# Kernel optimization log

Hardware: AMD Instinct MI355X
Metric: run time of the kernel (lower is better)

## Reference

```python
import jax, jax.numpy as jnp
import numpy as np

B, G, C, Hmlp, R = 4, 2048, 384, 1536, 96
NH = 6          # attention heads
V = 6           # number of 2D views (len(out_transform_2d))
NC = 1024       # number of clusters for segment_csr
GX = GY = 32    # grid shape per view
SCALE_FACTOR = 0.5  # args.scale_factor
COEF_PRO = 0.5      # args.coef_pro
EPS_LN = 1e-5
EPS_BN = 1e-5


def _forward(x, center1, norm1_g, norm1_b, qkv_w, proj_w, proj_b, norm2_g, norm2_b,
             fc1_w, fc1_b, fc2_w, fc2_b, ada1_w, ada1_b, ada2_w, ada2_b,
             bn3_g, bn3_b, bn3_m, bn3_v, bn2_g, bn2_b, bn2_m, bn2_v,
             norm3_g, norm3_b, a1_qkv_w, a1_proj_w, a1_proj_b,
             mask, idx_ptr, sorted_cluster_indices, cluster, flat_grid_index,
             grid_shape_x, grid_shape_y):
    B_, G1, C_ = x.shape
    hd = C_ // NH

    def ln(t, g, b):
        mu = t.mean(-1, keepdims=True)
        var = ((t - mu) ** 2).mean(-1, keepdims=True)
        return (t - mu) * jax.lax.rsqrt(var + EPS_LN) * g + b

    def bn_gelu(t, g, b, m, v):  # BatchNorm1d (eval) + GELU
        t = (t - m) * jax.lax.rsqrt(v + EPS_BN) * g + b
        return jax.nn.gelu(t, approximate=False)

    # ---- multi-head self-attention sublayer ----
    h = ln(x, norm1_g, norm1_b)
    qkv = (h @ qkv_w).reshape(B_, G1, 3, NH, hd).transpose(2, 0, 3, 1, 4)
    q, k, v = qkv[0], qkv[1], qkv[2]
    attn = jax.nn.softmax(jnp.einsum('bhqd,bhkd->bhqk', q, k) * hd ** -0.5, axis=-1)
    o = jnp.einsum('bhqk,bhkd->bhqd', attn, v).transpose(0, 2, 1, 3).reshape(B_, G1, C_)
    x = x + o @ proj_w + proj_b

    # ---- MLP + adapter sublayer ----
    h2 = ln(x, norm2_g, norm2_b)
    ffn = jax.nn.gelu(h2 @ fc1_w + fc1_b, approximate=False) @ fc2_w + fc2_b
    a = ffn @ ada1_w + ada1_b
    a = a * jax.nn.sigmoid(1.702 * a)      # QuickGELU
    ada = a @ ada2_w + ada2_b
    x = x + ffn + SCALE_FACTOR * ada

    cls_x = x[:, :1]
    pts = x[:, 1:]
    Gp = G1 - 1
    N = B_ * Gp

    # ---- 3D branch: segment_csr max/mean over clusters, gather back ----
    feat = pts.reshape(N, C_)
    fs = feat[sorted_cluster_indices]
    seg = cluster[sorted_cluster_indices]          # sorted segment ids (CSR order)
    nc = idx_ptr.shape[0] - 1
    cnt = jax.ops.segment_sum(jnp.ones((N,), feat.dtype), seg, nc)
    fsum = jax.ops.segment_sum(fs, seg, nc)
    fmax = jax.ops.segment_max(fs, seg, nc)
    fmax = jnp.where(cnt[:, None] > 0, fmax, 0.0)
    fmean = fsum / jnp.maximum(cnt, 1.0)[:, None]
    x3d = bn_gelu(fmax + fmean, bn3_g, bn3_b, bn3_m, bn3_v)[cluster].reshape(pts.shape)

    # ---- per-view 2D branch: masked attn + scatter_max/mean over grid cells ----
    dim_size = center1.shape[0] * grid_shape_x * grid_shape_y
    nviews = center1.shape[1]
    views = []
    for i in range(nviews):
        fx = pts.reshape(N, C_)
        h3 = ln(fx, norm3_g[i], norm3_b[i]).reshape(B_, Gp, C_)
        qkv1 = (h3 @ a1_qkv_w[i]).reshape(B_, Gp, 3, C_).transpose(2, 0, 1, 3)
        q1, k1, v1 = qkv1[0], qkv1[1], qkv1[2]
        s = jnp.einsum('bqd,bkd->bqk', q1, k1) * C_ ** -0.5
        s = jnp.where(mask[i][None], s, jnp.finfo(s.dtype).min)
        o1 = jnp.einsum('bqk,bkd->bqd', jax.nn.softmax(s, axis=-1), v1) @ a1_proj_w[i] + a1_proj_b[i]
        fx = o1.reshape(N, C_) + fx
        gi = flat_grid_index[i]
        gc = jax.ops.segment_sum(jnp.ones((N,), fx.dtype), gi, dim_size)
        gs = jax.ops.segment_sum(fx, gi, dim_size)
        gm = jax.ops.segment_max(fx, gi, dim_size)
        gm = jnp.where(gc[:, None] > 0, gm, 0.0)
        cell = bn_gelu(gs / jnp.maximum(gc, 1.0)[:, None] + gm,
                       bn2_g[i], bn2_b[i], bn2_m[i], bn2_v[i])
        views.append(cell[gi].reshape(pts.shape))

    # ---- cosine-similarity weighted fusion across views ----
    x_sup = jnp.stack(views, 0)                     # [V,B,G,C]
    dot = jnp.sum(x_sup * x3d[None], -1)
    nrm = jnp.linalg.norm(x_sup, axis=-1) * jnp.linalg.norm(x3d, axis=-1)[None]
    sims = (dot / jnp.maximum(nrm, 1e-8) + 1.0) / 2.0
    sims = sims / sims.sum(0, keepdims=True)
    x_sup_w = jnp.sum(x_sup * sims[..., None], 0)
    pts = pts + COEF_PRO * x_sup_w
    return jnp.concatenate([cls_x, pts], axis=1)


def setup_inputs() -> dict:
    rng = np.random.default_rng(0)
    key = jax.random.key(0)
    N = B * G
    # consistent cluster structure: every cluster non-empty
    cluster = np.concatenate([np.arange(NC), rng.integers(0, NC, N - NC)]).astype(np.int32)
    rng.shuffle(cluster)
    sorted_idx = np.argsort(cluster, kind='stable').astype(np.int32)
    counts = np.bincount(cluster, minlength=NC)
    idx_ptr = np.concatenate([[0], np.cumsum(counts)]).astype(np.int32)
    flat_grid_index = rng.integers(0, B * GX * GY, (V, N)).astype(np.int32)
    mask = (rng.random((V, G, G)) < 0.25) | np.eye(G, dtype=bool)[None]
    ks = jax.random.split(key, 16)
    f32 = jnp.float32
    def w(k, shape, s=0.02):
        return jax.random.normal(k, shape, f32) * s
    return {
        'x': jax.random.normal(ks[0], (B, G + 1, C), f32),
        'center1': jax.random.normal(ks[1], (B, V, G, 3), f32),
        'norm1_g': jnp.ones((C,), f32), 'norm1_b': jnp.zeros((C,), f32),
        'qkv_w': w(ks[2], (C, 3 * C)), 'proj_w': w(ks[3], (C, C)), 'proj_b': jnp.zeros((C,), f32),
        'norm2_g': jnp.ones((C,), f32), 'norm2_b': jnp.zeros((C,), f32),
        'fc1_w': w(ks[4], (C, Hmlp)), 'fc1_b': jnp.zeros((Hmlp,), f32),
        'fc2_w': w(ks[5], (Hmlp, C)), 'fc2_b': jnp.zeros((C,), f32),
        'ada1_w': w(ks[6], (C, R)), 'ada1_b': jnp.zeros((R,), f32),
        'ada2_w': w(ks[7], (R, C)), 'ada2_b': jnp.zeros((C,), f32),
        'bn3_g': jnp.ones((C,), f32), 'bn3_b': jnp.zeros((C,), f32),
        'bn3_m': w(ks[8], (C,), 0.1), 'bn3_v': jnp.ones((C,), f32) + jax.random.uniform(ks[9], (C,), f32) * 0.5,
        'bn2_g': jnp.ones((V, C), f32), 'bn2_b': jnp.zeros((V, C), f32),
        'bn2_m': w(ks[10], (V, C), 0.1), 'bn2_v': jnp.ones((V, C), f32) + jax.random.uniform(ks[11], (V, C), f32) * 0.5,
        'norm3_g': jnp.ones((V, C), f32), 'norm3_b': jnp.zeros((V, C), f32),
        'a1_qkv_w': w(ks[12], (V, C, 3 * C)), 'a1_proj_w': w(ks[13], (V, C, C)), 'a1_proj_b': jnp.zeros((V, C), f32),
        'mask': jnp.asarray(mask),
        'idx_ptr': jnp.asarray(idx_ptr),
        'sorted_cluster_indices': jnp.asarray(sorted_idx),
        'cluster': jnp.asarray(cluster),
        'flat_grid_index': jnp.asarray(flat_grid_index),
        'grid_shape_x': GX,
        'grid_shape_y': GY,
    }


def reference(x, center1, norm1_g, norm1_b, qkv_w, proj_w, proj_b, norm2_g, norm2_b,
              fc1_w, fc1_b, fc2_w, fc2_b, ada1_w, ada1_b, ada2_w, ada2_b,
              bn3_g, bn3_b, bn3_m, bn3_v, bn2_g, bn2_b, bn2_m, bn2_v,
              norm3_g, norm3_b, a1_qkv_w, a1_proj_w, a1_proj_b,
              mask, idx_ptr, sorted_cluster_indices, cluster, flat_grid_index,
              grid_shape_x, grid_shape_y):
    return _forward(x, center1, norm1_g, norm1_b, qkv_w, proj_w, proj_b, norm2_g, norm2_b,
                    fc1_w, fc1_b, fc2_w, fc2_b, ada1_w, ada1_b, ada2_w, ada2_b,
                    bn3_g, bn3_b, bn3_m, bn3_v, bn2_g, bn2_b, bn2_m, bn2_v,
                    norm3_g, norm3_b, a1_qkv_w, a1_proj_w, a1_proj_b,
                    mask, idx_ptr, sorted_cluster_indices, cluster, flat_grid_index,
                    grid_shape_x, grid_shape_y)
```

## Files before the change

### kernel.cpp

```cpp
#include <hip/hip_runtime.h>
#include <math.h>

typedef short bf16x8 __attribute__((ext_vector_type(8)));
typedef float f32x4 __attribute__((ext_vector_type(4)));

#define GLL16(g, l) \
  __builtin_amdgcn_global_load_lds((__attribute__((address_space(1))) const unsigned int*)(g), \
                                   (__attribute__((address_space(3))) unsigned int*)(l), 16, 0, 0)

__device__ __forceinline__ float wsum(float v){
  #pragma unroll
  for (int o=32;o;o>>=1) v += __shfl_xor(v,o);
  return v;
}
__device__ __forceinline__ float geluf(float x){
  return 0.5f*x*(1.0f+erff(x*0.7071067811865475f));
}
__device__ __forceinline__ short fbf(float f){
  unsigned u = __float_as_uint(f);
  unsigned r = (u + 0x7fffu + ((u>>16)&1u)) >> 16;
  return (short)r;
}
__device__ __forceinline__ float bff(short s){
  return __uint_as_float(((unsigned)(unsigned short)s)<<16);
}
__device__ __forceinline__ unsigned fkey(float f){
  unsigned b=__float_as_uint(f);
  return (b&0x80000000u)? ~b : (b|0x80000000u);
}
__device__ __forceinline__ float fdec(unsigned k){
  unsigned b=(k&0x80000000u)? (k&0x7fffffffu) : ~k;
  return __uint_as_float(b);
}

__global__ void mask_bits_kernel(const void* __restrict__ m, unsigned long long* __restrict__ mb,
                                 long long nOut, int mode){
  long long i = (long long)blockIdx.x*256 + threadIdx.x;
  if (i>=nOut) return;
  unsigned long long bits = 0;
  if (mode){
    const unsigned long long* p = (const unsigned long long*)((const unsigned char*)m + i*64);
    #pragma unroll
    for (int k=0;k<8;k++){
      unsigned long long v = p[k];
      #pragma unroll
      for (int b=0;b<8;b++)
        bits |= (unsigned long long)(((v>>(b*8))&0xffull)!=0) << (k*8+b);
    }
  } else {
    const int4* p = (const int4*)((const int*)m + i*64);
    #pragma unroll
    for (int k=0;k<16;k++){
      int4 v = p[k];
      bits |= (unsigned long long)(v.x!=0) << (k*4+0);
      bits |= (unsigned long long)(v.y!=0) << (k*4+1);
      bits |= (unsigned long long)(v.z!=0) << (k*4+2);
      bits |= (unsigned long long)(v.w!=0) << (k*4+3);
    }
  }
  mb[i] = bits;
}

__device__ __forceinline__ float epi(float v, const float* bias, int col, int act){
  if (bias) v += bias[col];
  if (act==1) v = geluf(v);
  else if (act==2) v = v*(1.f/(1.f+__expf(-1.702f*v)));
  return v;
}

#define XBM 128
#define XBN 128
#define XBK 32
__global__ __launch_bounds__(256)
void gemm_bf16_big(const short* __restrict__ A, int lda, long long sA,
                   const short* __restrict__ B, int ldb, long long sB,
                   const float* __restrict__ bias, long long sBias,
                   const float* __restrict__ res, int ldr, long long sR,
                   void* __restrict__ out, int ldo, long long sO, int outbf16,
                   int M, int N, int K, int act, int KS)
{
  __shared__ short As[XBM*XBK];
  __shared__ short Bs[XBN*XBK];
  int zz = blockIdx.z;
  int z = zz / KS, ks = zz - z*KS;
  A += (long long)z*sA; B += (long long)z*sB;
  if (res) res += (long long)z*sR;
  if (bias) bias += (long long)z*sBias;
  float* outF = (float*)out + (long long)z*sO;
  short* outH = (short*)out + (long long)z*sO;

  int tid = threadIdx.x;
  int rowBase = blockIdx.y*XBM;
  int colBase = blockIdx.x*XBN;

  int Kc = ((K + KS*XBK - 1)/(KS*XBK))*XBK;
  int kbeg = ks*Kc;
  int kend = min(K, kbeg+Kc);
  if (kbeg >= kend) return;

  int w = tid>>6;
  int lane = tid&63;
  int lm = lane&15, quad = lane>>4;
  int waveM = w>>1, waveN = w&1;

  int arow0 = min(rowBase + w*32 + lm,      M-1);
  int arow1 = min(rowBase + w*32 + 16 + lm, M-1);
  int brow0 = min(colBase + w*32 + lm,      N-1);
  int brow1 = min(colBase + w*32 + 16 + lm, N-1);
  const short* Ag0 = A + (long long)arow0*lda + quad*8;
  const short* Ag1 = A + (long long)arow1*lda + quad*8;
  const short* Bg0 = B + (long long)brow0*ldb + quad*8;
  const short* Bg1 = B + (long long)brow1*ldb + quad*8;
  short* Al0 = &As[(w*2+0)*512];
  short* Al1 = &As[(w*2+1)*512];
  short* Bl0 = &Bs[(w*2+0)*512];
  short* Bl1 = &Bs[(w*2+1)*512];

  f32x4 acc[4][4] = {};

  for (int k0=kbeg; k0<kend; k0+=XBK){
    GLL16(Ag0 + k0, Al0);
    GLL16(Ag1 + k0, Al1);
    GLL16(Bg0 + k0, Bl0);
    GLL16(Bg1 + k0, Bl1);
    __syncthreads();
    bf16x8 af[4], bfr[4];
    #pragma unroll
    for (int tm=0;tm<4;tm++) af[tm]  = *(bf16x8*)&As[(waveM*4+tm)*512 + quad*128 + lm*8];
    #pragma unroll
    for (int tn=0;tn<4;tn++) bfr[tn] = *(bf16x8*)&Bs[(waveN*4+tn)*512 + quad*128 + lm*8];
    #pragma unroll
    for (int tm=0;tm<4;tm++)
      #pragma unroll
      for (int tn=0;tn<4;tn++)
        acc[tm][tn] = __builtin_amdgcn_mfma_f32_16x16x32_bf16(af[tm], bfr[tn], acc[tm][tn], 0,0,0);
    __syncthreads();
  }

  #pragma unroll
  for (int tm=0;tm<4;tm++){
    #pragma unroll
    for (int tn=0;tn<4;tn++){
      int col = colBase + waveN*64 + tn*16 + lm;
      if (col>=N) continue;
      #pragma unroll
      for (int reg=0;reg<4;reg++){
        int row = rowBase + waveM*64 + tm*16 + quad*4 + reg;
        if (row>=M) continue;
        float v = acc[tm][tn][reg];
        if (KS>1){ atomicAdd(&outF[(long long)row*ldo+col], v); continue; }
        v = epi(v, bias, col, act);
        if (res) v += res[(long long)row*ldr+col];
        if (outbf16) outH[(long long)row*ldo+col] = fbf(v);
        else         outF[(long long)row*ldo+col] = v;
      }
    }
  }
}

__global__ __launch_bounds__(256)
void gemm_bf16_s(const short* __restrict__ A, int lda, long long sA,
                 const short* __restrict__ B, int ldb, long long sB,
                 const float* __restrict__ bias, long long sBias,
                 const float* __restrict__ res, int ldr, long long sR,
                 void* __restrict__ out, int ldo, long long sO, int outbf16,
                 int M, int N, int K, int act, short* __restrict__ out2,
                 const int* __restrict__ sgi, float* __restrict__ ssum,
                 unsigned* __restrict__ smax, float* __restrict__ scnt)
{
  __shared__ short As[64*32];
  __shared__ short Bs[64*32];
  int z = blockIdx.z;
  A += (long long)z*sA; B += (long long)z*sB;
  if (res) res += (long long)z*sR;
  if (bias) bias += (long long)z*sBias;
  float* outF = (float*)out + (long long)z*sO;
  short* outH = (short*)out + (long long)z*sO;

  int tid = threadIdx.x;
  int rowBase = blockIdx.y*64;
  int colBase = blockIdx.x*64;

  int w = tid>>6;
  int lane = tid&63;
  int lm = lane&15, quad = lane>>4;
  int wm = w>>1, wn = w&1;

  int arow = min(rowBase + w*16 + lm, M-1);
  int brow = min(colBase + w*16 + lm, N-1);
  const short* Ag = A + (long long)arow*lda + quad*8;
  const short* Bg = B + (long long)brow*ldb + quad*8;
  short* Al = &As[w*512];
  short* Bl = &Bs[w*512];

  f32x4 acc[2][2] = {};

  for (int k0=0; k0<K; k0+=32){
    GLL16(Ag + k0, Al);
    GLL16(Bg + k0, Bl);
    __syncthreads();
    bf16x8 af[2], bfr[2];
    #pragma unroll
    for (int tm=0;tm<2;tm++) af[tm]  = *(bf16x8*)&As[(wm*2+tm)*512 + quad*128 + lm*8];
    #pragma unroll
    for (int tn=0;tn<2;tn++) bfr[tn] = *(bf16x8*)&Bs[(wn*2+tn)*512 + quad*128 + lm*8];
    #pragma unroll
    for (int tm=0;tm<2;tm++)
      #pragma unroll
      for (int tn=0;tn<2;tn++)
        acc[tm][tn] = __builtin_amdgcn_mfma_f32_16x16x32_bf16(af[tm], bfr[tn], acc[tm][tn], 0,0,0);
    __syncthreads();
  }

  #pragma unroll
  for (int tm=0;tm<2;tm++){
    #pragma unroll
    for (int tn=0;tn<2;tn++){
      int col = colBase + wn*32 + tn*16 + lm;
      if (col>=N) continue;
      #pragma unroll
      for (int reg=0;reg<4;reg++){
        int row = rowBase + wm*32 + tm*16 + quad*4 + reg;
        if (row>=M) continue;
        float v = epi(acc[tm][tn][reg], bias, col, act);
        if (res) v += res[(long long)row*ldr+col];
        if (outbf16==3){
          int gi = sgi[(long long)z*8192 + row];
          long long base = ((long long)z*4096 + gi)*384 + col;
          atomicAdd(&ssum[base], v);
          atomicMax(&smax[base], fkey(v));
          if (col==0) atomicAdd(&scnt[(long long)z*4096 + gi], 1.0f);
        }
        else if (outbf16==2){
          int bb = row>>11;
          outH[((long long)bb*384 + col)*2048 + (row&2047)] = fbf(v);
        }
        else if (outbf16) outH[(long long)row*ldo+col] = fbf(v);
        else {
          outF[(long long)row*ldo+col] = v;
          if (out2) out2[(long long)row*ldo+col] = fbf(v);
        }
      }
    }
  }
}

__global__ __launch_bounds__(256,2)
void flash_view(const short* __restrict__ QK6, const short* __restrict__ Vt6,
                const unsigned long long* __restrict__ maskbits, short* __restrict__ O6)
{
  __shared__ char lds[58112];
  const float scale = 0.05103103630798288f;
  int id = blockIdx.x;
  int xcd = id & 7;
  int j = id >> 3;
  int vb = xcd*3 + (j>>5);
  int qt = j & 31;
  int v = vb >> 2, b = vb & 3;
  int tid=threadIdx.x, w=tid>>6, lane=tid&63, lm=lane&15, quad=lane>>4;

  const short* Qp = QK6 + ((long long)v*8192 + b*2048 + qt*64)*768;
  const short* Kp = QK6 + ((long long)v*8192 + b*2048)*768 + 384;
  const short* Vp = Vt6 + (long long)(v*4+b)*384*2048;
  const unsigned long long* Mb = maskbits + (long long)v*2048*32 + (long long)qt*64*32;
  short* Op = O6 + ((long long)v*8192 + b*2048 + qt*64)*384;

  short* P = (short*)(lds + 49152);
  float* alphaL = (float*)(lds + 57856);

  bf16x8 af[12];
  #pragma unroll
  for (int c=0;c<12;c++)
    af[c] = *(const bf16x8*)(Qp + (long long)(w*16+lm)*768 + c*32 + quad*8);

  float m_i[4], l_i[4];
  #pragma unroll
  for (int r=0;r<4;r++){ m_i[r]=-3.0e38f; l_i[r]=0.f; }
  f32x4 Oacc[4][6] = {};

  for (int kt=0; kt<32; kt++){
    #pragma unroll
    for (int c=0;c<12;c++)
      GLL16(Kp + (long long)(kt*64 + w*16 + lm)*768 + c*32 + quad*8, (short*)(lds + w*12288 + c*1024));
    __syncthreads();
    unsigned long long mb[4];
    #pragma unroll
    for (int r=0;r<4;r++)
      mb[r] = Mb[(long long)(w*16+quad*4+r)*32 + kt];
    f32x4 S[4];
    #pragma unroll
    for (int i=0;i<4;i++) S[i] = (f32x4){0.f,0.f,0.f,0.f};
    __builtin_amdgcn_s_setprio(1);
    #pragma unroll
    for (int kc=0;kc<12;kc++){
      #pragma unroll
      for (int ct=0;ct<4;ct++){
        bf16x8 bf = *(bf16x8*)(lds + ct*12288 + kc*1024 + quad*256 + lm*16);
        S[ct] = __builtin_amdgcn_mfma_f32_16x16x32_bf16(af[kc], bf, S[ct], 0,0,0);
      }
    }
    __builtin_amdgcn_s_setprio(0);
    #pragma unroll
    for (int r=0;r<4;r++){
      unsigned long long t = mb[r] >> lm;
      S[0][r] = ((unsigned)t      & 1u) ? S[0][r]*scale : -3.0e38f;
      S[1][r] = ((unsigned)(t>>16)& 1u) ? S[1][r]*scale : -3.0e38f;
      S[2][r] = ((unsigned)(t>>32)& 1u) ? S[2][r]*scale : -3.0e38f;
      S[3][r] = ((unsigned)(t>>48)& 1u) ? S[3][r]*scale : -3.0e38f;
    }
    float alpha[4], mnew[4];
    #pragma unroll
    for (int r=0;r<4;r++){
      float rm = S[0][r];
      #pragma unroll
      for (int ct=1;ct<4;ct++) rm = fmaxf(rm, S[ct][r]);
      #pragma unroll
      for (int o=1;o<16;o<<=1) rm = fmaxf(rm, __shfl_xor(rm, o));
      mnew[r] = fmaxf(m_i[r], rm);
      alpha[r] = __expf(m_i[r]-mnew[r]);
      m_i[r] = mnew[r];
    }
    float rs[4] = {0.f,0.f,0.f,0.f};
    #pragma unroll
    for (int ct=0;ct<4;ct++){
      #pragma unroll
      for (int r=0;r<4;r++){
        float sv = S[ct][r];
        float p = (sv > -1.0e37f) ? __expf(sv - mnew[r]) : 0.f;
        rs[r] += p;
        P[(w*16+quad*4+r)*68 + ct*16 + lm] = fbf(p);
      }
    }
    #pragma unroll
    for (int r=0;r<4;r++){
      #pragma unroll
      for (int o=1;o<16;o<<=1) rs[r] += __shfl_xor(rs[r], o);
      l_i[r] = l_i[r]*alpha[r] + rs[r];
    }
    if (lm==0){
      #pragma unroll
      for (int r=0;r<4;r++) alphaL[w*16+quad*4+r] = alpha[r];
    }
    bf16x8 Vreg[6][2];
    #pragma unroll
    for (int jj=0;jj<6;jj++)
      #pragma unroll
      for (int kk=0;kk<2;kk++)
        Vreg[jj][kk] = *(const bf16x8*)(Vp + (long long)((w*6+jj)*16+lm)*2048 + kt*64 + kk*32 + quad*8);
    __syncthreads();
    f32x4 am[4];
    #pragma unroll
    for (int m=0;m<4;m++) am[m] = *(f32x4*)&alphaL[m*16 + quad*4];
    #pragma unroll
    for (int m=0;m<4;m++)
      #pragma unroll
      for (int tn=0;tn<6;tn++)
        Oacc[m][tn] *= am[m];
    __builtin_amdgcn_s_setprio(1);
    #pragma unroll
    for (int kk=0;kk<2;kk++){
      bf16x8 ap[4];
      #pragma unroll
      for (int m=0;m<4;m++) ap[m] = *(bf16x8*)&P[(m*16+lm)*68 + kk*32 + quad*8];
      #pragma unroll
      for (int tn=0;tn<6;tn++){
        #pragma unroll
        for (int m=0;m<4;m++)
          Oacc[m][tn] = __builtin_amdgcn_mfma_f32_16x16x32_bf16(ap[m], Vreg[tn][kk], Oacc[m][tn], 0,0,0);
      }
    }
    __builtin_amdgcn_s_setprio(0);
  }

  __syncthreads();
  if (lm==0){
    #pragma unroll
    for (int r=0;r<4;r++) alphaL[w*16+quad*4+r] = l_i[r];
  }
  __syncthreads();
  f32x4 lv[4];
  #pragma unroll
  for (int m=0;m<4;m++) lv[m] = *(f32x4*)&alphaL[m*16 + quad*4];
  #pragma unroll
  for (int m=0;m<4;m++){
    #pragma unroll
    for (int tn=0;tn<6;tn++){
      #pragma unroll
      for (int reg=0;reg<4;reg++){
        Op[(long long)(m*16+quad*4+reg)*384 + (w*6+tn)*16 + lm] = fbf(Oacc[m][tn][reg] / lv[m][reg]);
      }
    }
  }
}

__global__ __launch_bounds__(256,3)
void flash_inner(const short* __restrict__ QKV, const short* __restrict__ Vt,
                 short* __restrict__ O)
{
  __shared__ char lds[33536];
  int id = blockIdx.x;
  int xcd = id & 7;
  int j = id >> 3;
  int bh = xcd*3 + j/33;
  int qt = j%33;
  int b=bh/6, h=bh-b*6;
  int tid=threadIdx.x, w=tid>>6, lane=tid&63, lm=lane&15, quad=lane>>4;

  const short* Qb = QKV + (long long)b*2049*1152 + h*64;
  const short* Kb = Qb + 384;
  const short* Vtp = Vt + (long long)bh*64*2176;
  short* Op = O + ((long long)b*2049 + qt*64)*384 + h*64;

  short* P = (short*)(lds + 16384);
  float* alphaL = (float*)(lds + 33280);

  int qr = min(qt*64 + w*16 + lm, 2048);
  bf16x8 af[2];
  #pragma unroll
  for (int c=0;c<2;c++)
    af[c] = *(const bf16x8*)(Qb + (long long)qr*1152 + c*32 + quad*8);

  float m_i[4], l_i[4];
  #pragma unroll
  for (int r=0;r<4;r++){ m_i[r]=-3.0e38f; l_i[r]=0.f; }
  f32x4 Oacc[4] = {};

  #pragma unroll
  for (int h2=0;h2<2;h2++){
    int kr0 = min((w*2+h2)*16 + lm, 2048);
    #pragma unroll
    for (int c=0;c<2;c++)
      GLL16(Kb + (long long)kr0*1152 + c*32 + quad*8, (short*)(lds + (w*2+h2)*2048 + c*1024));
  }

  for (int kt=0; kt<17; kt++){
    __syncthreads();
    f32x4 S[8];
    #pragma unroll
    for (int i=0;i<8;i++) S[i] = (f32x4){0.f,0.f,0.f,0.f};
    __builtin_amdgcn_s_setprio(1);
    #pragma unroll
    for (int kc=0;kc<2;kc++){
      #pragma unroll
      for (int ct=0;ct<8;ct++){
        bf16x8 bf = *(bf16x8*)(lds + ct*2048 + kc*1024 + quad*256 + lm*16);
        S[ct] = __builtin_amdgcn_mfma_f32_16x16x32_bf16(af[kc], bf, S[ct], 0,0,0);
      }
    }
    __builtin_amdgcn_s_setprio(0);
    #pragma unroll
    for (int ct=0;ct<8;ct++){
      int scol = kt*128 + ct*16 + lm;
      bool ok = scol <= 2048;
      #pragma unroll
      for (int r=0;r<4;r++) S[ct][r] = ok ? S[ct][r]*0.125f : -3.0e38f;
    }
    float alpha[4], mnew[4];
    #pragma unroll
    for (int r=0;r<4;r++){
      float rm = S[0][r];
      #pragma unroll
      for (int ct=1;ct<8;ct++) rm = fmaxf(rm, S[ct][r]);
      #pragma unroll
      for (int o=1;o<16;o<<=1) rm = fmaxf(rm, __shfl_xor(rm, o));
      mnew[r] = fmaxf(m_i[r], rm);
      alpha[r] = __expf(m_i[r]-mnew[r]);
      m_i[r] = mnew[r];
    }
    float rs[4] = {0.f,0.f,0.f,0.f};
    #pragma unroll
    for (int ct=0;ct<8;ct++){
      #pragma unroll
      for (int r=0;r<4;r++){
        float sv = S[ct][r];
        float p = (sv > -1.0e37f) ? __expf(sv - mnew[r]) : 0.f;
        rs[r] += p;
        P[(w*16+quad*4+r)*132 + ct*16 + lm] = fbf(p);
      }
    }
    #pragma unroll
    for (int r=0;r<4;r++){
      #pragma unroll
      for (int o=1;o<16;o<<=1) rs[r] += __shfl_xor(rs[r], o);
      l_i[r] = l_i[r]*alpha[r] + rs[r];
    }
    if (lm==0){
      #pragma unroll
      for (int r=0;r<4;r++) alphaL[w*16+quad*4+r] = alpha[r];
    }
    bf16x8 Vreg[4];
    #pragma unroll
    for (int kk=0;kk<4;kk++)
      Vreg[kk] = *(const bf16x8*)(Vtp + (long long)(w*16+lm)*2176 + kt*128 + kk*32 + quad*8);
    __syncthreads();
    if (kt < 16){
      #pragma unroll
      for (int h2=0;h2<2;h2++){
        int krn = min((kt+1)*128 + (w*2+h2)*16 + lm, 2048);
        #pragma unroll
        for (int c=0;c<2;c++)
          GLL16(Kb + (long long)krn*1152 + c*32 + quad*8, (short*)(lds + (w*2+h2)*2048 + c*1024));
      }
    }
    f32x4 am[4];
    #pragma unroll
    for (int m=0;m<4;m++) am[m] = *(f32x4*)&alphaL[m*16 + quad*4];
    #pragma unroll
    for (int m=0;m<4;m++) Oacc[m] *= am[m];
    __builtin_amdgcn_s_setprio(1);
    #pragma unroll
    for (int kk=0;kk<4;kk++){
      bf16x8 ap[4];
      #pragma unroll
      for (int m=0;m<4;m++) ap[m] = *(bf16x8*)&P[(m*16+lm)*132 + kk*32 + quad*8];
      #pragma unroll
      for (int m=0;m<4;m++)
        Oacc[m] = __builtin_amdgcn_mfma_f32_16x16x32_bf16(ap[m], Vreg[kk], Oacc[m], 0,0,0);
    }
    __builtin_amdgcn_s_setprio(0);
  }

  __syncthreads();
  if (lm==0){
    #pragma unroll
    for (int r=0;r<4;r++) alphaL[w*16+quad*4+r] = l_i[r];
  }
  __syncthreads();
  f32x4 lv[4];
  #pragma unroll
  for (int m=0;m<4;m++) lv[m] = *(f32x4*)&alphaL[m*16 + quad*4];
  #pragma unroll
  for (int m=0;m<4;m++){
    #pragma unroll
    for (int reg=0;reg<4;reg++){
      int row = qt*64 + m*16 + quad*4 + reg;
      if (row < 2049)
        Op[(long long)(m*16+quad*4+reg)*384 + w*16 + lm] = fbf(Oacc[m][reg] / lv[m][reg]);
    }
  }
}

__global__ __launch_bounds__(128)
void ln_bf16_kernel(const float* __restrict__ in, const float* __restrict__ g,
                    const float* __restrict__ bt, short* __restrict__ out)
{
  long long row = blockIdx.x;
  const float* p = in + row*384;
  int tid = threadIdx.x;
  float v0=p[tid], v1=p[tid+128], v2=p[tid+256];
  float s = v0+v1+v2;
  float ss = v0*v0+v1*v1+v2*v2;
  __shared__ float r1[2], r2[2];
  s = wsum(s); ss = wsum(ss);
  int wid=tid>>6, lane=tid&63;
  if (lane==0){ r1[wid]=s; r2[wid]=ss; }
  __syncthreads();
  float mean=(r1[0]+r1[1])*(1.f/384.f);
  float var =(r2[0]+r2[1])*(1.f/384.f)-mean*mean;
  float rstd=rsqrtf(var+1e-5f);
  short* o = out + row*384;
  o[tid]     = fbf((v0-mean)*rstd*g[tid]+bt[tid]);
  o[tid+128] = fbf((v1-mean)*rstd*g[tid+128]+bt[tid+128]);
  o[tid+256] = fbf((v2-mean)*rstd*g[tid+256]+bt[tid+256]);
}

__global__ __launch_bounds__(128)
void ln6_kernel(const float* __restrict__ in, const float* __restrict__ g6,
                const float* __restrict__ b6, short* __restrict__ out6)
{
  long long row = blockIdx.x;
  const float* p = in + row*384;
  int tid = threadIdx.x;
  float v0=p[tid], v1=p[tid+128], v2=p[tid+256];
  float s = v0+v1+v2;
  float ss = v0*v0+v1*v1+v2*v2;
  __shared__ float r1[2], r2[2];
  s = wsum(s); ss = wsum(ss);
  int wid=tid>>6, lane=tid&63;
  if (lane==0){ r1[wid]=s; r2[wid]=ss; }
  __syncthreads();
  float mean=(r1[0]+r1[1])*(1.f/384.f);
  float var =(r2[0]+r2[1])*(1.f/384.f)-mean*mean;
  float rstd=rsqrtf(var+1e-5f);
  float n0=(v0-mean)*rstd, n1=(v1-mean)*rstd, n2=(v2-mean)*rstd;
  #pragma unroll
  for (int i=0;i<6;i++){
    const float* g = g6 + i*384;
    const float* bt = b6 + i*384;
    short* o = out6 + (long long)i*8192*384 + row*384;
    o[tid]     = fbf(n0*g[tid]+bt[tid]);
    o[tid+128] = fbf(n1*g[tid+128]+bt[tid+128]);
    o[tid+256] = fbf(n2*g[tid+256]+bt[tid+256]);
  }
}

__global__ __launch_bounds__(256)
void tconv_kernel(const float* __restrict__ in, int ldin, long long sIn, long long sIn2, int zmod,
                  int R, int C, short* __restrict__ out, int ldout, long long sOut)
{
  __shared__ float tile[32][33];
  int z = blockIdx.z;
  const float* ip = in + (long long)(z/zmod)*sIn + (long long)(z%zmod)*sIn2;
  short* op = out + (long long)z*sOut;
  int r0 = blockIdx.x*32;
  int c0 = blockIdx.y*32;
  int tx = threadIdx.x&31, ty = threadIdx.x>>5;
  #pragma unroll
  for (int i=0;i<4;i++){
    int r = r0 + ty + i*8, c = c0 + tx;
    tile[ty+i*8][tx] = (r<R && c<C) ? ip[(long long)r*ldin + c] : 0.f;
  }
  __syncthreads();
  #pragma unroll
  for (int i=0;i<4;i++){
    int oc = c0 + ty + i*8;
    int orr = r0 + tx;
    if (oc<C && orr<ldout) op[(long long)oc*ldout + orr] = fbf(tile[tx][ty+i*8]);
  }
}

__global__ __launch_bounds__(256)
void tconv16_kernel(const short* __restrict__ in, int ldin, long long sIn, long long sIn2, int zmod,
                    int R, int C, short* __restrict__ out, int ldout, long long sOut)
{
  __shared__ short tile[32][34];
  int z = blockIdx.z;
  const short* ip = in + (long long)(z/zmod)*sIn + (long long)(z%zmod)*sIn2;
  short* op = out + (long long)z*sOut;
  int r0 = blockIdx.x*32;
  int c0 = blockIdx.y*32;
  int tx = threadIdx.x&31, ty = threadIdx.x>>5;
  #pragma unroll
  for (int i=0;i<4;i++){
    int r = r0 + ty + i*8, c = c0 + tx;
    tile[ty+i*8][tx] = (r<R && c<C) ? ip[(long long)r*ldin + c] : (short)0;
  }
  __syncthreads();
  #pragma unroll
  for (int i=0;i<4;i++){
    int oc = c0 + ty + i*8;
    int orr = r0 + tx;
    if (oc<C && orr<ldout) op[(long long)oc*ldout + orr] = tile[tx][ty+i*8];
  }
}

__global__ void ew_fuse_kernel(const float* __restrict__ x1, const float* __restrict__ ffn,
                               const float* __restrict__ ada,
                               const int* __restrict__ cluster,
                               float* __restrict__ fsum, unsigned* __restrict__ fmax,
                               float* __restrict__ cnt,
                               float* __restrict__ ptsb, float* __restrict__ out){
  long long i=(long long)blockIdx.x*256+threadIdx.x;
  if (i >= 8196ll*384) return;
  float v = x1[i] + ffn[i] + 0.5f*ada[i];
  long long row = i/384; int c = (int)(i - row*384);
  long long b = row/2049; long long g = row - b*2049;
  if (g == 0){ out[b*2049*384 + c] = v; return; }
  long long n = b*2048 + (g-1);
  ptsb[n*384 + c] = v;
  int s = cluster[n];
  atomicAdd(&fsum[(long long)s*384 + c], v);
  atomicMax(&fmax[(long long)s*384 + c], fkey(v));
  if (c==0) atomicAdd(&cnt[s], 1.0f);
}

__global__ __launch_bounds__(128)
void cell_kernel(const float* __restrict__ fsum, const unsigned* __restrict__ fmax,
                 const float* __restrict__ cnt,
                 const float* __restrict__ g, const float* __restrict__ bb,
                 const float* __restrict__ m, const float* __restrict__ v,
                 float* __restrict__ out, long long zSum, long long zCnt, long long zP)
{
  int s = blockIdx.x, z = blockIdx.y;
  fsum += (long long)z*zSum; fmax += (long long)z*zSum; cnt += (long long)z*zCnt;
  g += (long long)z*zP; bb += (long long)z*zP; m += (long long)z*zP; v += (long long)z*zP;
  out += (long long)z*zSum;
  float cn = cnt[s];
  float denom = fmaxf(cn, 1.f);
  int tid = threadIdx.x;
  #pragma unroll
  for (int k=0;k<3;k++){
    int c = tid + k*128;
    float mx = (cn>0.f) ? fdec(fmax[(long long)s*384+c]) : 0.f;
    float t = mx + fsum[(long long)s*384+c]/denom;
    t = (t - m[c])*rsqrtf(v[c]+1e-5f)*g[c] + bb[c];
    out[(long long)s*384+c] = geluf(t);
  }
}

__global__ __launch_bounds__(384)
void combine_kernel(const float* __restrict__ pts, const float* __restrict__ cell3,
                    const int* __restrict__ cluster, const float* __restrict__ cell2,
                    const int* __restrict__ gidx, float* __restrict__ out)
{
  int n = blockIdx.x;
  int tid = threadIdx.x;
  int w = tid>>6, lane = tid&63;
  __shared__ float sdot[6], ssq[6], sn3s;
  __shared__ int soff[6];
  const float* x3 = cell3 + (long long)cluster[n]*384;
  int gi = gidx[(long long)w*8192 + n];
  const float* r = cell2 + ((long long)w*4096 + gi)*384;
  float d=0.f, s2=0.f, q3=0.f;
  #pragma unroll
  for (int k=0;k<6;k++){
    int c = lane + k*64;
    float a = r[c], x = x3[c];
    d += a*x; s2 += a*a; q3 += x*x;
  }
  d = wsum(d); s2 = wsum(s2); q3 = wsum(q3);
  if (lane==0){ sdot[w]=d; ssq[w]=s2; soff[w]=gi; if (w==0) sn3s=q3; }
  __syncthreads();
  float sn3 = sqrtf(sn3s);
  float sims[6]; float ssumv=0.f;
  #pragma unroll
  for (int i=0;i<6;i++){
    float nrm = sqrtf(ssq[i])*sn3;
    float s = (sdot[i]/fmaxf(nrm,1e-8f) + 1.f)*0.5f;
    sims[i]=s; ssumv+=s;
  }
  int c = tid;
  float acc=0.f;
  #pragma unroll
  for (int i=0;i<6;i++){
    const float* rr = cell2 + ((long long)i*4096 + soff[i])*384;
    acc += (sims[i]/ssumv)*rr[c];
  }
  int b = n>>11, gp = n&2047;
  out[((long long)(b*2049 + 1 + gp))*384 + c] = pts[(long long)n*384+c] + 0.5f*acc;
}

static inline void launch_gemm16b(hipStream_t s, const short* A,int lda,long long sA,
  const short* B,int ldb,long long sB, const float* bias, long long sBias,
  const float* res,int ldr,long long sR, void* out,int ldo,long long sO,int outbf16,
  int M,int N,int K,int act,int nz,int KS)
{
  dim3 g((N+XBN-1)/XBN,(M+XBM-1)/XBM,(unsigned)(nz*KS));
  hipLaunchKernelGGL(gemm_bf16_big,g,dim3(256),0,s,
    A,lda,sA,B,ldb,sB,bias,sBias,res,ldr,sR,out,ldo,sO,outbf16,M,N,K,act,KS);
}
static inline void launch_gemm16s(hipStream_t s, const short* A,int lda,long long sA,
  const short* B,int ldb,long long sB, const float* bias, long long sBias,
  const float* res,int ldr,long long sR, void* out,int ldo,long long sO,int outbf16,
  int M,int N,int K,int act,int nz, short* out2=nullptr,
  const int* sgi=nullptr, float* ssum=nullptr, unsigned* smax=nullptr, float* scnt=nullptr)
{
  dim3 g((N+63)/64,(M+63)/64,(unsigned)nz);
  hipLaunchKernelGGL(gemm_bf16_s,g,dim3(256),0,s,
    A,lda,sA,B,ldb,sB,bias,sBias,res,ldr,sR,out,ldo,sO,outbf16,M,N,K,act,out2,
    sgi,ssum,smax,scnt);
}
static inline void launch_tconv(hipStream_t s, const float* in,int ldin,long long sIn,long long sIn2,int zmod,
  int R,int C, short* out,int ldout,long long sOut,int nz)
{
  dim3 g((ldout+31)/32,(C+31)/32,(unsigned)nz);
  hipLaunchKernelGGL(tconv_kernel,g,dim3(256),0,s, in,ldin,sIn,sIn2,zmod,R,C,out,ldout,sOut);
}
static inline void launch_tconv16(hipStream_t s, const short* in,int ldin,long long sIn,long long sIn2,int zmod,
  int R,int C, short* out,int ldout,long long sOut,int nz)
{
  dim3 g((ldout+31)/32,(C+31)/32,(unsigned)nz);
  hipLaunchKernelGGL(tconv16_kernel,g,dim3(256),0,s, in,ldin,sIn,sIn2,zmod,R,C,out,ldout,sOut);
}

extern "C" void kernel_launch(void* const* d_in, const int* in_sizes, int n_in,
                              void* d_out, int out_size, void* d_ws, size_t ws_size,
                              hipStream_t stream)
{
  const float* x       = (const float*)d_in[0];
  const float* norm1_g = (const float*)d_in[2];
  const float* norm1_b = (const float*)d_in[3];
  const float* qkv_w   = (const float*)d_in[4];
  const float* proj_w  = (const float*)d_in[5];
  const float* proj_b  = (const float*)d_in[6];
  const float* norm2_g = (const float*)d_in[7];
  const float* norm2_b = (const float*)d_in[8];
  const float* fc1_w   = (const float*)d_in[9];
  const float* fc1_b   = (const float*)d_in[10];
  const float* fc2_w   = (const float*)d_in[11];
  const float* fc2_b   = (const float*)d_in[12];
  const float* ada1_w  = (const float*)d_in[13];
  const float* ada1_b  = (const float*)d_in[14];
  const float* ada2_w  = (const float*)d_in[15];
  const float* ada2_b  = (const float*)d_in[16];
  const float* bn3_g   = (const float*)d_in[17];
  const float* bn3_b   = (const float*)d_in[18];
  const float* bn3_m   = (const float*)d_in[19];
  const float* bn3_v   = (const float*)d_in[20];
  const float* bn2_g   = (const float*)d_in[21];
  const float* bn2_b   = (const float*)d_in[22];
  const float* bn2_m   = (const float*)d_in[23];
  const float* bn2_v   = (const float*)d_in[24];
  const float* norm3_g = (const float*)d_in[25];
  const float* norm3_b = (const float*)d_in[26];
  const float* a1_qkv_w  = (const float*)d_in[27];
  const float* a1_proj_w = (const float*)d_in[28];
  const float* a1_proj_b = (const float*)d_in[29];
  const void*  maskp     = d_in[30];
  const int*   cluster   = (const int*)d_in[33];
  const int*   fgi       = (const int*)d_in[34];
  float* out = (float*)d_out;

  size_t off = 0;
  char* wsb = (char*)d_ws;
  auto alloc = [&](size_t bytes)->void*{
    void* p = wsb + off;
    off += (bytes + 255) & ~(size_t)255;
    return p;
  };
  short*    bufHh = (short*)alloc(8196ll*384*2);
  float*    ptsb  = (float*)alloc(8192ll*384*4);
  float*    cnt   = (float*)alloc(1024*4);
  float*    fsum  = (float*)alloc(1024ll*384*4);
  unsigned* fmaxe = (unsigned*)alloc(1024ll*384*4);
  float*    cell3 = (float*)alloc(1024ll*384*4);
  unsigned char* maskb = (unsigned char*)alloc(6ll*2048*2048);
  float*    gc6   = (float*)alloc(6ll*4096*4);
  short*    qkvT  = (short*)alloc(1152ll*384*2);
  short*    projT = (short*)alloc(384ll*384*2);
  short*    fc1T  = (short*)alloc(1536ll*384*2);
  short*    fc2T  = (short*)alloc(384ll*1536*2);
  short*    ada1T = (short*)alloc(96ll*384*2);
  short*    ada2T = (short*)alloc(384ll*96*2);
  short*    a1qkvT  = (short*)alloc(6ll*1152*384*2);
  short*    a1projT = (short*)alloc(6ll*384*384*2);
  int*      flag  = (int*)alloc(256);
  char* arena = (char*)alloc(188743680);
  char* A0 = arena;
  char* A1 = arena + 75497472;
  char* A2 = arena + 150994944;
  short* bufQh = (short*)(A0 + 0);
  float* bufO  = (float*)(A0 + 20971520);
  short* bufOh = (short*)(A0 + 35651584);
  short* bufAh = (short*)(A0 + 44040192);
  float* bufX  = (float*)(A0 + 46137344);
  float* bufAda= (float*)(A0 + 0);
  short* Vt_i  = (short*)(A1 + 0);
  short* bufTh = (short*)(A1 + 8388608);
  short* QK6   = (short*)(A0 + 0);
  short* Vt6   = (short*)(A1 + 0);
  short* O6    = (short*)(A2 + 0);
  short* bufHh6= (short*)(A2 + 0);
  float* gsum6 = (float*)(A1 + 0);
  unsigned* gmaxe6 = (unsigned*)(A1 + 37748736);
  float* cell2 = (float*)(A0 + 0);

  unsigned long long* maskbits = (unsigned long long*)maskb;

  {
    int mode = (in_sizes[30] == 6*2048*2048) ? 1 : 0;
    long long nOut = 6ll*2048*32;
    mask_bits_kernel<<<dim3((unsigned)((nOut+255)/256)),dim3(256),0,stream>>>(maskp, maskbits, nOut, mode);
  }

  launch_tconv(stream, qkv_w, 1152, 0,0,1, 384,1152, qkvT, 384, 0, 1);
  launch_tconv(stream, proj_w, 384, 0,0,1, 384,384,  projT, 384, 0, 1);
  launch_tconv(stream, fc1_w, 1536, 0,0,1, 384,1536, fc1T, 384, 0, 1);
  launch_tconv(stream, fc2_w, 384,  0,0,1, 1536,384, fc2T, 1536, 0, 1);
  launch_tconv(stream, ada1_w, 96,  0,0,1, 384,96,   ada1T, 384, 0, 1);
  launch_tconv(stream, ada2_w, 384, 0,0,1, 96,384,   ada2T, 96, 0, 1);
  launch_tconv(stream, a1_qkv_w, 1152, 384ll*1152,0,1, 384,1152, a1qkvT, 384, 1152ll*384, 6);
  launch_tconv(stream, a1_proj_w, 384, 384ll*384,0,1, 384,384,  a1projT, 384, 384ll*384, 6);

  ln_bf16_kernel<<<8196,128,0,stream>>>(x, norm1_g, norm1_b, bufHh);
  launch_gemm16b(stream, bufHh,384,0, qkvT,384,0, nullptr,0, nullptr,0,0,
                 bufQh,1152,0,1, 8196,1152,384, 0, 1,1);
  launch_tconv16(stream, bufQh + 768, 1152, 2049ll*1152, 64, 6, 2049, 64, Vt_i, 2176, 64ll*2176, 24);
  flash_inner<<<dim3(792),256,0,stream>>>(bufQh, Vt_i, bufOh);
  launch_gemm16s(stream, bufOh,384,0, projT,384,0, proj_b,0, x,384,0,
                 bufX,384,0,0, 8196,384,384, 0, 1);
  ln_bf16_kernel<<<8196,128,0,stream>>>(bufX, norm2_g, norm2_b, bufHh);
  launch_gemm16b(stream, bufHh,384,0, fc1T,384,0, fc1_b,0, nullptr,0,0,
                 bufTh,1536,0,1, 8196,1536,384, 1, 1,1);
  launch_gemm16s(stream, bufTh,1536,0, fc2T,1536,0, fc2_b,0, nullptr,0,0,
                 bufO,384,0,0, 8196,384,1536, 0, 1, bufOh);
  launch_gemm16s(stream, bufOh,384,0, ada1T,384,0, ada1_b,0, nullptr,0,0,
                 bufAh,96,0,1, 8196,96,384, 2, 1);
  launch_gemm16s(stream, bufAh,96,0, ada2T,96,0, ada2_b,0, nullptr,0,0,
                 bufAda,384,0,0, 8196,384,96, 0, 1);
  hipMemsetAsync(cnt, 0, 4096 + 2*1572864, stream);
  ew_fuse_kernel<<<dim3((unsigned)((8196ll*384+255)/256)),256,0,stream>>>(
      bufX, bufO, bufAda, cluster, fsum, fmaxe, cnt, ptsb, out);

  cell_kernel<<<dim3(1024,1),128,0,stream>>>(fsum, fmaxe, cnt, bn3_g,bn3_b,bn3_m,bn3_v, cell3, 0,0,0);

  ln6_kernel<<<8192,128,0,stream>>>(ptsb, norm3_g, norm3_b, bufHh6);
  launch_gemm16b(stream, bufHh6,384,8192ll*384, a1qkvT,384,1152ll*384,
                 nullptr,0, nullptr,0,0, QK6,768,8192ll*768,1, 8192,768,384, 0, 6,1);
  launch_gemm16s(stream, bufHh6,384,8192ll*384, a1qkvT + 768ll*384,384,1152ll*384,
                 nullptr,0, nullptr,0,0, Vt6,2048,4ll*384*2048,2, 8192,384,384, 0, 6);

  flash_view<<<dim3(768),256,0,stream>>>(QK6, Vt6, maskbits, O6);

  hipMemsetAsync(gsum6, 0, 2ll*37748736, stream);
  hipMemsetAsync(gc6, 0, 6ll*4096*4, stream);
  launch_gemm16s(stream, O6,384,8192ll*384, a1projT,384,384ll*384,
                 a1_proj_b,384, ptsb,384,0,
                 nullptr,384,0,3, 8192,384,384, 0, 6, nullptr,
                 fgi, gsum6, gmaxe6, gc6);
  cell_kernel<<<dim3(4096,6),128,0,stream>>>(gsum6, gmaxe6, gc6,
      bn2_g, bn2_b, bn2_m, bn2_v, cell2, 4096ll*384, 4096, 384);

  combine_kernel<<<8192,384,0,stream>>>(ptsb, cell3, cluster, cell2, fgi, out);
}
```

Measured before the change: 1.423 ms.

## Deepen small-GEMM K step and compute V-transpose GEMM with swapped operands

The small GEMM kernel now stages 64 K elements per iteration instead of 32, halving the number of barrier/load rounds. To keep K a multiple of 64, the adapter bottleneck is padded from 96 to 128, with a memset to zero the padded activation buffer and a wider transposed weight. The V projection for the view attention is rewritten as weights × activations with a per-z A divisor, so the transposed layout is produced by ordinary row-major stores instead of scattered transposed writes. This adds an extra memset, doubles LDS use per block and relies on the padded weight columns being zero.

```diff
diff --git a/kernel.cpp b/kernel.cpp
--- a/kernel.cpp
+++ b/kernel.cpp
@@ -159,7 +159,7 @@
 }
 
 __global__ __launch_bounds__(256)
-void gemm_bf16_s(const short* __restrict__ A, int lda, long long sA,
+void gemm_bf16_s(const short* __restrict__ A, int lda, long long sA, int aDiv,
                  const short* __restrict__ B, int ldb, long long sB,
                  const float* __restrict__ bias, long long sBias,
                  const float* __restrict__ res, int ldr, long long sR,
@@ -168,10 +168,10 @@
                  const int* __restrict__ sgi, float* __restrict__ ssum,
                  unsigned* __restrict__ smax, float* __restrict__ scnt)
 {
-  __shared__ short As[64*32];
-  __shared__ short Bs[64*32];
+  __shared__ short As[64*64];
+  __shared__ short Bs[64*64];
   int z = blockIdx.z;
-  A += (long long)z*sA; B += (long long)z*sB;
+  A += (long long)(z/aDiv)*sA; B += (long long)z*sB;
   if (res) res += (long long)z*sR;
   if (bias) bias += (long long)z*sBias;
   float* outF = (float*)out + (long long)z*sO;
@@ -190,25 +190,30 @@
   int brow = min(colBase + w*16 + lm, N-1);
   const short* Ag = A + (long long)arow*lda + quad*8;
   const short* Bg = B + (long long)brow*ldb + quad*8;
-  short* Al = &As[w*512];
-  short* Bl = &Bs[w*512];
+  short* Al = &As[w*1024];
+  short* Bl = &Bs[w*1024];
 
   f32x4 acc[2][2] = {};
 
-  for (int k0=0; k0<K; k0+=32){
-    GLL16(Ag + k0, Al);
-    GLL16(Bg + k0, Bl);
+  for (int k0=0; k0<K; k0+=64){
+    GLL16(Ag + k0,      Al);
+    GLL16(Ag + k0 + 32, Al + 512);
+    GLL16(Bg + k0,      Bl);
+    GLL16(Bg + k0 + 32, Bl + 512);
     __syncthreads();
-    bf16x8 af[2], bfr[2];
-    #pragma unroll
-    for (int tm=0;tm<2;tm++) af[tm]  = *(bf16x8*)&As[(wm*2+tm)*512 + quad*128 + lm*8];
-    #pragma unroll
-    for (int tn=0;tn<2;tn++) bfr[tn] = *(bf16x8*)&Bs[(wn*2+tn)*512 + quad*128 + lm*8];
-    #pragma unroll
-    for (int tm=0;tm<2;tm++)
-      #pragma unroll
-      for (int tn=0;tn<2;tn++)
-        acc[tm][tn] = __builtin_amdgcn_mfma_f32_16x16x32_bf16(af[tm], bfr[tn], acc[tm][tn], 0,0,0);
+    #pragma unroll
+    for (int kc=0;kc<2;kc++){
+      bf16x8 af[2], bfr[2];
+      #pragma unroll
+      for (int tm=0;tm<2;tm++) af[tm]  = *(bf16x8*)&As[(wm*2+tm)*1024 + kc*512 + quad*128 + lm*8];
+      #pragma unroll
+      for (int tn=0;tn<2;tn++) bfr[tn] = *(bf16x8*)&Bs[(wn*2+tn)*1024 + kc*512 + quad*128 + lm*8];
+      #pragma unroll
+      for (int tm=0;tm<2;tm++)
+        #pragma unroll
+        for (int tn=0;tn<2;tn++)
+          acc[tm][tn] = __builtin_amdgcn_mfma_f32_16x16x32_bf16(af[tm], bfr[tn], acc[tm][tn], 0,0,0);
+    }
     __syncthreads();
   }
 
@@ -230,10 +235,6 @@
           atomicAdd(&ssum[base], v);
           atomicMax(&smax[base], fkey(v));
           if (col==0) atomicAdd(&scnt[(long long)z*4096 + gi], 1.0f);
-        }
-        else if (outbf16==2){
-          int bb = row>>11;
-          outH[((long long)bb*384 + col)*2048 + (row&2047)] = fbf(v);
         }
         else if (outbf16) outH[(long long)row*ldo+col] = fbf(v);
         else {
@@ -739,7 +740,7 @@
   hipLaunchKernelGGL(gemm_bf16_big,g,dim3(256),0,s,
     A,lda,sA,B,ldb,sB,bias,sBias,res,ldr,sR,out,ldo,sO,outbf16,M,N,K,act,KS);
 }
-static inline void launch_gemm16s(hipStream_t s, const short* A,int lda,long long sA,
+static inline void launch_gemm16s(hipStream_t s, const short* A,int lda,long long sA,int aDiv,
   const short* B,int ldb,long long sB, const float* bias, long long sBias,
   const float* res,int ldr,long long sR, void* out,int ldo,long long sO,int outbf16,
   int M,int N,int K,int act,int nz, short* out2=nullptr,
@@ -747,7 +748,7 @@
 {
   dim3 g((N+63)/64,(M+63)/64,(unsigned)nz);
   hipLaunchKernelGGL(gemm_bf16_s,g,dim3(256),0,s,
-    A,lda,sA,B,ldb,sB,bias,sBias,res,ldr,sR,out,ldo,sO,outbf16,M,N,K,act,out2,
+    A,lda,sA,aDiv,B,ldb,sB,bias,sBias,res,ldr,sR,out,ldo,sO,outbf16,M,N,K,act,out2,
     sgi,ssum,smax,scnt);
 }
 static inline void launch_tconv(hipStream_t s, const float* in,int ldin,long long sIn,long long sIn2,int zmod,
@@ -821,7 +822,7 @@
   short*    fc1T  = (short*)alloc(1536ll*384*2);
   short*    fc2T  = (short*)alloc(384ll*1536*2);
   short*    ada1T = (short*)alloc(96ll*384*2);
-  short*    ada2T = (short*)alloc(384ll*96*2);
+  short*    ada2T = (short*)alloc(384ll*128*2);
   short*    a1qkvT  = (short*)alloc(6ll*1152*384*2);
   short*    a1projT = (short*)alloc(6ll*384*384*2);
   int*      flag  = (int*)alloc(256);
@@ -833,7 +834,7 @@
   float* bufO  = (float*)(A0 + 20971520);
   short* bufOh = (short*)(A0 + 35651584);
   short* bufAh = (short*)(A0 + 44040192);
-  float* bufX  = (float*)(A0 + 46137344);
+  float* bufX  = (float*)(A0 + 46399488);
   float* bufAda= (float*)(A0 + 0);
   short* Vt_i  = (short*)(A1 + 0);
   short* bufTh = (short*)(A1 + 8388608);
@@ -858,7 +859,7 @@
   launch_tconv(stream, fc1_w, 1536, 0,0,1, 384,1536, fc1T, 384, 0, 1);
   launch_tconv(stream, fc2_w, 384,  0,0,1, 1536,384, fc2T, 1536, 0, 1);
   launch_tconv(stream, ada1_w, 96,  0,0,1, 384,96,   ada1T, 384, 0, 1);
-  launch_tconv(stream, ada2_w, 384, 0,0,1, 96,384,   ada2T, 96, 0, 1);
+  launch_tconv(stream, ada2_w, 384, 0,0,1, 96,384,   ada2T, 128, 0, 1);
   launch_tconv(stream, a1_qkv_w, 1152, 384ll*1152,0,1, 384,1152, a1qkvT, 384, 1152ll*384, 6);
   launch_tconv(stream, a1_proj_w, 384, 384ll*384,0,1, 384,384,  a1projT, 384, 384ll*384, 6);
 
@@ -867,17 +868,18 @@
                  bufQh,1152,0,1, 8196,1152,384, 0, 1,1);
   launch_tconv16(stream, bufQh + 768, 1152, 2049ll*1152, 64, 6, 2049, 64, Vt_i, 2176, 64ll*2176, 24);
   flash_inner<<<dim3(792),256,0,stream>>>(bufQh, Vt_i, bufOh);
-  launch_gemm16s(stream, bufOh,384,0, projT,384,0, proj_b,0, x,384,0,
+  launch_gemm16s(stream, bufOh,384,0,1, projT,384,0, proj_b,0, x,384,0,
                  bufX,384,0,0, 8196,384,384, 0, 1);
   ln_bf16_kernel<<<8196,128,0,stream>>>(bufX, norm2_g, norm2_b, bufHh);
   launch_gemm16b(stream, bufHh,384,0, fc1T,384,0, fc1_b,0, nullptr,0,0,
                  bufTh,1536,0,1, 8196,1536,384, 1, 1,1);
-  launch_gemm16s(stream, bufTh,1536,0, fc2T,1536,0, fc2_b,0, nullptr,0,0,
+  launch_gemm16s(stream, bufTh,1536,0,1, fc2T,1536,0, fc2_b,0, nullptr,0,0,
                  bufO,384,0,0, 8196,384,1536, 0, 1, bufOh);
-  launch_gemm16s(stream, bufOh,384,0, ada1T,384,0, ada1_b,0, nullptr,0,0,
-                 bufAh,96,0,1, 8196,96,384, 2, 1);
-  launch_gemm16s(stream, bufAh,96,0, ada2T,96,0, ada2_b,0, nullptr,0,0,
-                 bufAda,384,0,0, 8196,384,96, 0, 1);
+  hipMemsetAsync(bufAh, 0, 8196ll*128*2, stream);
+  launch_gemm16s(stream, bufOh,384,0,1, ada1T,384,0, ada1_b,0, nullptr,0,0,
+                 bufAh,128,0,1, 8196,96,384, 2, 1);
+  launch_gemm16s(stream, bufAh,128,0,1, ada2T,128,0, ada2_b,0, nullptr,0,0,
+                 bufAda,384,0,0, 8196,384,128, 0, 1);
   hipMemsetAsync(cnt, 0, 4096 + 2*1572864, stream);
   ew_fuse_kernel<<<dim3((unsigned)((8196ll*384+255)/256)),256,0,stream>>>(
       bufX, bufO, bufAda, cluster, fsum, fmaxe, cnt, ptsb, out);
@@ -887,14 +889,15 @@
   ln6_kernel<<<8192,128,0,stream>>>(ptsb, norm3_g, norm3_b, bufHh6);
   launch_gemm16b(stream, bufHh6,384,8192ll*384, a1qkvT,384,1152ll*384,
                  nullptr,0, nullptr,0,0, QK6,768,8192ll*768,1, 8192,768,384, 0, 6,1);
-  launch_gemm16s(stream, bufHh6,384,8192ll*384, a1qkvT + 768ll*384,384,1152ll*384,
-                 nullptr,0, nullptr,0,0, Vt6,2048,4ll*384*2048,2, 8192,384,384, 0, 6);
+  launch_gemm16s(stream, a1qkvT + 768ll*384,384,1152ll*384,4,
+                 bufHh6,384,2048ll*384, nullptr,0, nullptr,0,0,
+                 Vt6,2048,384ll*2048,1, 384,2048,384, 0, 24);
 
   flash_view<<<dim3(768),256,0,stream>>>(QK6, Vt6, maskbits, O6);
 
   hipMemsetAsync(gsum6, 0, 2ll*37748736, stream);
   hipMemsetAsync(gc6, 0, 6ll*4096*4, stream);
-  launch_gemm16s(stream, O6,384,8192ll*384, a1projT,384,384ll*384,
+  launch_gemm16s(stream, O6,384,8192ll*384,1, a1projT,384,384ll*384,
                  a1_proj_b,384, ptsb,384,0,
                  nullptr,384,0,3, 8192,384,384, 0, 6, nullptr,
                  fgi, gsum6, gmaxe6, gc6);
```

Result: faster. 1.393 ms (median of 4 runs) (-2.2%).
